# Kernel tuning notes

Measured on AMD Instinct MI355X. Metric: run time of the kernel, lower is better.

## Reference

```python
import jax, jax.numpy as jnp
import numpy as np

N, H, B = 8192, 32, 256
AVG_DEG = 32.0


def setup_inputs() -> dict:
    key = jax.random.key(0)
    ks = jax.random.split(key, 16)
    z = jax.random.normal(ks[0], (N, H), jnp.float32)
    # binary adjacency with ~AVG_DEG neighbors per node; S = row-normalized A
    A = (jax.random.uniform(ks[1], (N, N)) < (AVG_DEG / N)).astype(jnp.float32)
    deg = A.sum(1, keepdims=True)
    S = jnp.where(deg > 0, A / jnp.maximum(deg, 1.0), 0.0)
    u_idx = jax.random.randint(ks[2], (B,), 0, N, dtype=jnp.int32)
    v_idx = jax.random.randint(ks[3], (B,), 0, N, dtype=jnp.int32)
    k = jax.random.randint(ks[4], (B,), 0, 2, dtype=jnp.int32)
    time_delta = jax.random.uniform(ks[5], (B, 2, 4), jnp.float32)

    def lin(kk, o, i):  # xavier-ish init
        return jax.random.normal(kk, (o, i), jnp.float32) * (1.0 / np.sqrt(i))

    return dict(
        z=z, A=A, S=S, u_idx=u_idx, v_idx=v_idx, k=k, time_delta=time_delta,
        W_h_w=lin(ks[6], H, H), W_h_b=jnp.zeros(H, jnp.float32),
        W_struct_w=lin(ks[7], H, H), W_struct_b=jnp.zeros(H, jnp.float32),
        W_rec_w=lin(ks[8], H, H), W_rec_b=jnp.zeros(H, jnp.float32),
        W_t_w=lin(ks[9], H, 4), W_t_b=jnp.zeros(H, jnp.float32),
        om0_w=lin(ks[10], 1, 2 * H), om0_b=jnp.zeros(1, jnp.float32),
        om1_w=lin(ks[11], 1, 2 * H), om1_b=jnp.zeros(1, jnp.float32),
        psi=0.5 * jnp.ones(2, jnp.float32),
    )


def reference(z, A, S, u_idx, v_idx, k, time_delta,
              W_h_w, W_h_b, W_struct_w, W_struct_b,
              W_rec_w, W_rec_b, W_t_w, W_t_b,
              om0_w, om0_b, om1_w, om1_b, psi):
    kpos = k > 0  # [B]

    # ---- intensity_rate_lambda (non-bilinear g_fn, edge_type=None) ----
    zu, zv = z[u_idx], z[v_idx]                      # [B,H]
    cat_uv = jnp.concatenate([zu, zv], axis=1)       # [B,2H]
    cat_vu = jnp.concatenate([zv, zu], axis=1)

    def g_fn(zc):  # selects omega[0] for k<=0, omega[1] for k>0
        g0 = (zc @ om0_w.T + om0_b)[:, 0]
        g1 = (zc @ om1_w.T + om1_b)[:, 0]
        return jnp.where(kpos, g1, g0)

    g = 0.5 * (g_fn(cat_uv) + g_fn(cat_vu))          # [B]
    psi_k = psi[kpos.astype(jnp.int32)]
    g_psi = jnp.clip(g / (psi_k + 1e-7), -75.0, 75.0)
    Lambda = psi_k * (jnp.log1p(jnp.exp(-g_psi)) + g_psi)

    # ---- update_node_embed: S-weighted neighbor aggregation + RNN-style update ----
    h_all = z @ W_h_w.T + W_h_b                      # W_h(z) for all nodes [N,H]
    targets = jnp.stack([u_idx, v_idx], axis=1)      # nodes being updated [B,2]
    partners = jnp.stack([v_idx, u_idx], axis=1)     # struct comes from partner

    mask = A[partners] > 0                           # [B,2,N] neighbor mask
    q = jnp.exp(S[partners]) * mask                  # attention over neighbors
    q = q / (q.sum(-1, keepdims=True) + 1e-7)
    sig = jax.nn.sigmoid(q[..., None] * h_all[None, None])   # [B,2,N,H]
    h_struct = jnp.where(mask[..., None], sig, -jnp.inf).max(axis=2)  # [B,2,H]
    has_nb = mask.any(-1, keepdims=True)
    h_struct = jnp.where(has_nb, h_struct, 0.0)

    h1 = h_struct @ W_struct_w.T + W_struct_b        # [B,2,H]
    z_new = jax.nn.sigmoid(h1 + z[targets] @ W_rec_w.T + W_rec_b
                           + time_delta @ W_t_w.T + W_t_b)  # [B,2,H]
    return Lambda, z_new
```

## Files before the change

kernel.cpp:

```cpp
#include <hip/hip_runtime.h>
#include <hip/hip_bf16.h>
#include <math.h>

#define H 32
#define MAXNBR 512
#define CHUNK 64

__global__ __launch_bounds__(256) void fused_kernel(
    const float* __restrict__ S,
    const float* __restrict__ z,
    const int* __restrict__ u_idx, const int* __restrict__ v_idx,
    const int* __restrict__ k,
    const float* __restrict__ time_delta,
    const float* __restrict__ W_h_w, const float* __restrict__ W_h_b,
    const float* __restrict__ W_struct_w, const float* __restrict__ W_struct_b,
    const float* __restrict__ W_rec_w, const float* __restrict__ W_rec_b,
    const float* __restrict__ W_t_w, const float* __restrict__ W_t_b,
    const float* __restrict__ om0_w, const float* __restrict__ om0_b,
    const float* __restrict__ om1_w, const float* __restrict__ om1_b,
    const float* __restrict__ psi,
    float* __restrict__ out_lambda,
    float* __restrict__ out_znew,
    int N)
{
    int pair = blockIdx.x;
    int b = pair >> 1;
    int j = pair & 1;
    int u = u_idx[b], v = v_idx[b];
    int target  = (j == 0) ? u : v;
    int partner = (j == 0) ? v : u;

    __shared__ float WshT[H * H];
    __shared__ float Bsh[H];
    __shared__ int   s_cnt;
    __shared__ float s_red[256];
    __shared__ int   s_nbr[MAXNBR];
    __shared__ float s_eq[MAXNBR];
    __shared__ float zsh[CHUNK][H];
    __shared__ float s_max[8][H];
    __shared__ float s_hstruct[H];

    int tid = threadIdx.x;
    if (tid == 0) s_cnt = 0;
    for (int i = tid; i < H * H; i += 256) {
        int hh = i >> 5, jj = i & 31;
        WshT[jj * H + hh] = W_h_w[i];
    }
    if (tid < H) Bsh[tid] = W_h_b[tid];

    if (j == 0 && tid == 255) {
        bool kpos = k[b] > 0;
        const float* om_w = kpos ? om1_w : om0_w;
        float om_bias = kpos ? om1_b[0] : om0_b[0];
        const float* zu = z + (size_t)u * H;
        const float* zv = z + (size_t)v * H;
        float g = 0.f;
#pragma unroll
        for (int hh = 0; hh < H; hh++)
            g += (om_w[hh] + om_w[hh + H]) * (zu[hh] + zv[hh]);
        g = 0.5f * g + om_bias;
        float psi_k = psi[kpos ? 1 : 0];
        float gp = g / (psi_k + 1e-7f);
        gp = fminf(fmaxf(gp, -75.f), 75.f);
        out_lambda[b] = psi_k * (log1pf(expf(-gp)) + gp);
    }
    __syncthreads();

    const float4* Srow4 = (const float4*)(S + (size_t)partner * N);
    float psum = 0.f;
    int n4 = N >> 2;
    for (int it = tid; it < n4; it += 256) {
        float4 sv = Srow4[it];
        const float* svp = &sv.x;
#pragma unroll
        for (int c = 0; c < 4; c++) {
            float s = svp[c];
            if (s > 0.f) {
                float e = expf(s);
                int pos = atomicAdd(&s_cnt, 1);
                if (pos < MAXNBR) { s_nbr[pos] = it * 4 + c; s_eq[pos] = e; }
                psum += e;
            }
        }
    }
    s_red[tid] = psum;
    __syncthreads();
    for (int s = 128; s > 0; s >>= 1) {
        if (tid < s) s_red[tid] += s_red[tid + s];
        __syncthreads();
    }
    float inv_qsum = 1.f / (s_red[0] + 1e-7f);
    int cnt = s_cnt;
    if (cnt > MAXNBR) cnt = MAXNBR;

    int grp = tid >> 5;
    int h   = tid & 31;
    float mmax = -INFINITY;
    for (int base = 0; base < cnt; base += CHUNK) {
        int m = min(CHUNK, cnt - base);
        for (int t = tid; t < m * 8; t += 256) {
            int i = t >> 3, c = t & 7;
            ((float4*)zsh[i])[c] =
                ((const float4*)(z + (size_t)s_nbr[base + i] * H))[c];
        }
        __syncthreads();
        for (int i = grp; i < m; i += 8) {
            float q = s_eq[base + i] * inv_qsum;
            float hv = Bsh[h];
#pragma unroll
            for (int jj = 0; jj < H; jj++)
                hv += WshT[jj * H + h] * zsh[i][jj];
            float sg = 1.f / (1.f + expf(-q * hv));
            mmax = fmaxf(mmax, sg);
        }
        __syncthreads();
    }
    s_max[grp][h] = mmax;
    __syncthreads();
    if (tid < H) {
        float mm = s_max[0][tid];
#pragma unroll
        for (int g = 1; g < 8; g++) mm = fmaxf(mm, s_max[g][tid]);
        s_hstruct[tid] = (cnt > 0) ? mm : 0.f;
    }
    __syncthreads();

    if (tid < H) {
        int hh = tid;
        float acc = W_struct_b[hh] + W_rec_b[hh] + W_t_b[hh];
        const float* zt = z + (size_t)target * H;
#pragma unroll
        for (int jj = 0; jj < H; jj++) {
            acc += W_struct_w[hh * H + jj] * s_hstruct[jj];
            acc += W_rec_w[hh * H + jj] * zt[jj];
        }
        const float* td = time_delta + (size_t)pair * 4;
#pragma unroll
        for (int jj = 0; jj < 4; jj++) acc += W_t_w[hh * 4 + jj] * td[jj];
        out_znew[(size_t)pair * H + hh] = 1.f / (1.f + expf(-acc));
    }
}

extern "C" void kernel_launch(void* const* d_in, const int* in_sizes, int n_in,
                              void* d_out, int out_size, void* d_ws, size_t ws_size,
                              hipStream_t stream) {
    const float* z          = (const float*)d_in[0];
    const float* S          = (const float*)d_in[2];
    const int*   u_idx      = (const int*)d_in[3];
    const int*   v_idx      = (const int*)d_in[4];
    const int*   k          = (const int*)d_in[5];
    const float* time_delta = (const float*)d_in[6];
    const float* W_h_w      = (const float*)d_in[7];
    const float* W_h_b      = (const float*)d_in[8];
    const float* W_struct_w = (const float*)d_in[9];
    const float* W_struct_b = (const float*)d_in[10];
    const float* W_rec_w    = (const float*)d_in[11];
    const float* W_rec_b    = (const float*)d_in[12];
    const float* W_t_w      = (const float*)d_in[13];
    const float* W_t_b      = (const float*)d_in[14];
    const float* om0_w      = (const float*)d_in[15];
    const float* om0_b      = (const float*)d_in[16];
    const float* om1_w      = (const float*)d_in[17];
    const float* om1_b      = (const float*)d_in[18];
    const float* psi        = (const float*)d_in[19];

    const int B = in_sizes[3];
    const int N = in_sizes[0] / H;
    float* out        = (float*)d_out;
    float* out_lambda = out;
    float* out_znew   = out + B;

    fused_kernel<<<B * 2, 256, 0, stream>>>(
        S, z, u_idx, v_idx, k, time_delta,
        W_h_w, W_h_b, W_struct_w, W_struct_b, W_rec_w, W_rec_b, W_t_w, W_t_b,
        om0_w, om0_b, om1_w, om1_b, psi,
        out_lambda, out_znew, N);
}
```

Measured before the change: 15.50 us.

## Prefetch S row into registers early and use wavefront shuffle reduction

```diff
diff --git a/kernel.cpp b/kernel.cpp
--- a/kernel.cpp
+++ b/kernel.cpp
@@ -33,7 +33,7 @@
     __shared__ float WshT[H * H];
     __shared__ float Bsh[H];
     __shared__ int   s_cnt;
-    __shared__ float s_red[256];
+    __shared__ float s_wred[4];
     __shared__ int   s_nbr[MAXNBR];
     __shared__ float s_eq[MAXNBR];
     __shared__ float zsh[CHUNK][H];
@@ -42,6 +42,16 @@
 
     int tid = threadIdx.x;
     if (tid == 0) s_cnt = 0;
+
+    const float4* Srow4 = (const float4*)(S + (size_t)partner * N);
+    int n4 = N >> 2;
+    bool fast = (n4 == 2048);
+    float4 sv[8];
+    if (fast) {
+#pragma unroll
+        for (int r = 0; r < 8; r++) sv[r] = Srow4[tid + r * 256];
+    }
+
     for (int i = tid; i < H * H; i += 256) {
         int hh = i >> 5, jj = i & 31;
         WshT[jj * H + hh] = W_h_w[i];
@@ -66,30 +76,46 @@
     }
     __syncthreads();
 
-    const float4* Srow4 = (const float4*)(S + (size_t)partner * N);
     float psum = 0.f;
-    int n4 = N >> 2;
-    for (int it = tid; it < n4; it += 256) {
-        float4 sv = Srow4[it];
-        const float* svp = &sv.x;
-#pragma unroll
-        for (int c = 0; c < 4; c++) {
-            float s = svp[c];
-            if (s > 0.f) {
-                float e = expf(s);
-                int pos = atomicAdd(&s_cnt, 1);
-                if (pos < MAXNBR) { s_nbr[pos] = it * 4 + c; s_eq[pos] = e; }
-                psum += e;
+    if (fast) {
+#pragma unroll
+        for (int r = 0; r < 8; r++) {
+            const float* svp = (const float*)&sv[r];
+#pragma unroll
+            for (int c = 0; c < 4; c++) {
+                float s = svp[c];
+                if (s > 0.f) {
+                    float e = expf(s);
+                    int pos = atomicAdd(&s_cnt, 1);
+                    if (pos < MAXNBR) {
+                        s_nbr[pos] = (tid + r * 256) * 4 + c;
+                        s_eq[pos] = e;
+                    }
+                    psum += e;
+                }
             }
         }
-    }
-    s_red[tid] = psum;
-    __syncthreads();
-    for (int s = 128; s > 0; s >>= 1) {
-        if (tid < s) s_red[tid] += s_red[tid + s];
-        __syncthreads();
-    }
-    float inv_qsum = 1.f / (s_red[0] + 1e-7f);
+    } else {
+        for (int it = tid; it < n4; it += 256) {
+            float4 s4 = Srow4[it];
+            const float* svp = (const float*)&s4;
+#pragma unroll
+            for (int c = 0; c < 4; c++) {
+                float s = svp[c];
+                if (s > 0.f) {
+                    float e = expf(s);
+                    int pos = atomicAdd(&s_cnt, 1);
+                    if (pos < MAXNBR) { s_nbr[pos] = it * 4 + c; s_eq[pos] = e; }
+                    psum += e;
+                }
+            }
+        }
+    }
+#pragma unroll
+    for (int off = 32; off > 0; off >>= 1) psum += __shfl_xor(psum, off);
+    if ((tid & 63) == 0) s_wred[tid >> 6] = psum;
+    __syncthreads();
+    float inv_qsum = 1.f / (s_wred[0] + s_wred[1] + s_wred[2] + s_wred[3] + 1e-7f);
     int cnt = s_cnt;
     if (cnt > MAXNBR) cnt = MAXNBR;
 
```

Measured after the change: 14.33 us. 7.5% less time.

## Widen blocks to 1024 threads, preload S row, use wave-aggregated atomics and shuffles

Applied to the files above, without the earlier changes.

```diff
diff --git a/kernel.cpp b/kernel.cpp
--- a/kernel.cpp
+++ b/kernel.cpp
@@ -3,10 +3,12 @@
 #include <math.h>
 
 #define H 32
-#define MAXNBR 512
-#define CHUNK 64
+#define NT 1024
+#define NW (NT / 64)
+#define NGRP (NT / 32)
+#define MAXNBR 1024
 
-__global__ __launch_bounds__(256) void fused_kernel(
+__global__ __launch_bounds__(NT) void fused_kernel(
     const float* __restrict__ S,
     const float* __restrict__ z,
     const int* __restrict__ u_idx, const int* __restrict__ v_idx,
@@ -33,22 +35,27 @@
     __shared__ float WshT[H * H];
     __shared__ float Bsh[H];
     __shared__ int   s_cnt;
-    __shared__ float s_red[256];
+    __shared__ float s_wred[NW];
     __shared__ int   s_nbr[MAXNBR];
     __shared__ float s_eq[MAXNBR];
-    __shared__ float zsh[CHUNK][H];
-    __shared__ float s_max[8][H];
+    __shared__ float s_max[NGRP][H];
     __shared__ float s_hstruct[H];
 
     int tid = threadIdx.x;
+    int lane = tid & 63;
     if (tid == 0) s_cnt = 0;
-    for (int i = tid; i < H * H; i += 256) {
-        int hh = i >> 5, jj = i & 31;
-        WshT[jj * H + hh] = W_h_w[i];
-    }
+
+    const float4* Srow4 = (const float4*)(S + (size_t)partner * N);
+    int n4 = N >> 2;
+    bool fast = (n4 == 2 * NT);
+    float4 sv0, sv1;
+    if (fast) { sv0 = Srow4[tid]; sv1 = Srow4[tid + NT]; }
+
+    for (int i = tid; i < H * H; i += NT)
+        WshT[(i & 31) * H + (i >> 5)] = W_h_w[i];
     if (tid < H) Bsh[tid] = W_h_b[tid];
 
-    if (j == 0 && tid == 255) {
+    if (j == 0 && tid == NT - 1) {
         bool kpos = k[b] > 0;
         const float* om_w = kpos ? om1_w : om0_w;
         float om_bias = kpos ? om1_b[0] : om0_b[0];
@@ -66,61 +73,70 @@
     }
     __syncthreads();
 
-    const float4* Srow4 = (const float4*)(S + (size_t)partner * N);
     float psum = 0.f;
-    int n4 = N >> 2;
-    for (int it = tid; it < n4; it += 256) {
-        float4 sv = Srow4[it];
-        const float* svp = &sv.x;
-#pragma unroll
-        for (int c = 0; c < 4; c++) {
-            float s = svp[c];
-            if (s > 0.f) {
-                float e = expf(s);
-                int pos = atomicAdd(&s_cnt, 1);
-                if (pos < MAXNBR) { s_nbr[pos] = it * 4 + c; s_eq[pos] = e; }
-                psum += e;
+    auto process = [&](float s, int n) {
+        float e = expf(s);
+        bool nb = s > 0.f;
+        psum += nb ? e : 0.f;
+        unsigned long long mask = __ballot(nb);
+        if (mask) {
+            int leader = (int)__ffsll((long long)mask) - 1;
+            int basec = 0;
+            if (lane == leader) basec = atomicAdd(&s_cnt, (int)__popcll(mask));
+            basec = __shfl(basec, leader, 64);
+            if (nb) {
+                int pos = basec + (int)__popcll(mask & ((1ull << lane) - 1ull));
+                if (pos < MAXNBR) { s_nbr[pos] = n; s_eq[pos] = e; }
             }
         }
+    };
+
+    if (fast) {
+        const float* p0 = (const float*)&sv0;
+        const float* p1 = (const float*)&sv1;
+#pragma unroll
+        for (int c = 0; c < 4; c++) process(p0[c], 4 * tid + c);
+#pragma unroll
+        for (int c = 0; c < 4; c++) process(p1[c], 4 * (tid + NT) + c);
+    } else {
+        for (int it = tid; it < n4; it += NT) {
+            float4 s4 = Srow4[it];
+            const float* sp = (const float*)&s4;
+#pragma unroll
+            for (int c = 0; c < 4; c++) process(sp[c], 4 * it + c);
+        }
     }
-    s_red[tid] = psum;
+
+#pragma unroll
+    for (int off = 32; off > 0; off >>= 1) psum += __shfl_xor(psum, off, 64);
+    if (lane == 0) s_wred[tid >> 6] = psum;
     __syncthreads();
-    for (int s = 128; s > 0; s >>= 1) {
-        if (tid < s) s_red[tid] += s_red[tid + s];
-        __syncthreads();
-    }
-    float inv_qsum = 1.f / (s_red[0] + 1e-7f);
+    float qs = 1e-7f;
+#pragma unroll
+    for (int w = 0; w < NW; w++) qs += s_wred[w];
+    float inv_qsum = 1.f / qs;
     int cnt = s_cnt;
     if (cnt > MAXNBR) cnt = MAXNBR;
 
     int grp = tid >> 5;
     int h   = tid & 31;
     float mmax = -INFINITY;
-    for (int base = 0; base < cnt; base += CHUNK) {
-        int m = min(CHUNK, cnt - base);
-        for (int t = tid; t < m * 8; t += 256) {
-            int i = t >> 3, c = t & 7;
-            ((float4*)zsh[i])[c] =
-                ((const float4*)(z + (size_t)s_nbr[base + i] * H))[c];
-        }
-        __syncthreads();
-        for (int i = grp; i < m; i += 8) {
-            float q = s_eq[base + i] * inv_qsum;
-            float hv = Bsh[h];
+    for (int i = grp; i < cnt; i += NGRP) {
+        float q = s_eq[i] * inv_qsum;
+        float zval = z[(size_t)s_nbr[i] * H + h];
+        float hv = Bsh[h];
 #pragma unroll
-            for (int jj = 0; jj < H; jj++)
-                hv += WshT[jj * H + h] * zsh[i][jj];
-            float sg = 1.f / (1.f + expf(-q * hv));
-            mmax = fmaxf(mmax, sg);
-        }
-        __syncthreads();
+        for (int jj = 0; jj < H; jj++)
+            hv += WshT[jj * H + h] * __shfl(zval, jj, 32);
+        float sg = 1.f / (1.f + expf(-q * hv));
+        mmax = fmaxf(mmax, sg);
     }
     s_max[grp][h] = mmax;
     __syncthreads();
     if (tid < H) {
         float mm = s_max[0][tid];
 #pragma unroll
-        for (int g = 1; g < 8; g++) mm = fmaxf(mm, s_max[g][tid]);
+        for (int g = 1; g < NGRP; g++) mm = fmaxf(mm, s_max[g][tid]);
         s_hstruct[tid] = (cnt > 0) ? mm : 0.f;
     }
     __syncthreads();
@@ -170,7 +186,7 @@
     float* out_lambda = out;
     float* out_znew   = out + B;
 
-    fused_kernel<<<B * 2, 256, 0, stream>>>(
+    fused_kernel<<<B * 2, NT, 0, stream>>>(
         S, z, u_idx, v_idx, k, time_delta,
         W_h_w, W_h_b, W_struct_w, W_struct_b, W_rec_w, W_rec_b, W_t_w, W_t_b,
         om0_w, om0_b, om1_w, om1_b, psi,
```

New measurement: 20.74 us. 33.8% more time.
